# Kernel optimization log

Measured on AMD Instinct MI355X. Metric: run time of the kernel, lower is better.

The kernel has to match this reference:

```python
import jax, jax.numpy as jnp
import numpy as np

T, N, E = 4, 50000, 800000
F, H, C_HID, C_OUT = 256, 128, 512, 2
SLOPE = 11.0 / 48.0  # torch RReLU eval-mode slope = (1/8 + 1/3) / 2


def _topk_pool(x, scorer, k):
    # x: [N, d], scorer: [d, 1] -> [d, k]
    scores = (x @ scorer) / jnp.maximum(jnp.linalg.norm(scorer), 1e-6)  # [N, 1]
    _, idx = jax.lax.top_k(scores[:, 0], k)
    return (x[idx] * jnp.tanh(scores[idx])).T


def _gru_cell(prev_Q, z, Wu, Uu, bu, Wr, Ur, br, Wh, Uh, bh):
    u = jax.nn.sigmoid(Wu @ z + Uu @ prev_Q + bu)
    r = jax.nn.sigmoid(Wr @ z + Ur @ prev_Q + br)
    h_cap = jnp.tanh(Wh @ z + Uh @ (r * prev_Q) + bh)
    return (1.0 - u) * prev_Q + u * h_cap


def _gcn_conv(x, src, dst, W):
    ones = jnp.ones(src.shape[0], x.dtype)
    deg_out = jnp.clip(jax.ops.segment_sum(ones, src, num_segments=N), 1.0)
    deg_in = jnp.clip(jax.ops.segment_sum(ones, dst, num_segments=N), 1.0)
    h = (x * (deg_out ** -0.5)[:, None]) @ W          # project first (out <= in)
    agg = jax.ops.segment_sum(h[src], dst, num_segments=N)
    out = agg * (deg_in ** -0.5)[:, None]
    return jnp.where(out >= 0, out, SLOPE * out)      # RReLU (eval mode)


def setup_inputs() -> dict:
    key = jax.random.key(0)
    ks = jax.random.split(key, 32)
    s = 0.05
    d = {}
    d['feats'] = jax.random.normal(ks[0], (T, N, F), jnp.float32)
    d['edges'] = jax.random.randint(ks[1], (T, 2, E), 0, N)
    d['scorer0'] = jax.random.normal(ks[2], (F, 1), jnp.float32) * s
    d['scorer1'] = jax.random.normal(ks[3], (H, 1), jnp.float32) * s
    d['gcn_W0'] = jax.random.normal(ks[4], (F, H), jnp.float32) * s
    d['gcn_W1'] = jax.random.normal(ks[5], (H, H), jnp.float32) * s
    i = 6
    for g in ('u', 'r', 'h'):
        d[g + '_W0'] = jax.random.normal(ks[i], (F, F), jnp.float32) * s; i += 1
        d[g + '_U0'] = jax.random.normal(ks[i], (F, F), jnp.float32) * s; i += 1
        d[g + '_b0'] = jax.random.normal(ks[i], (F, H), jnp.float32) * s; i += 1
    for g in ('u', 'r', 'h'):
        d[g + '_W1'] = jax.random.normal(ks[i], (H, H), jnp.float32) * s; i += 1
        d[g + '_U1'] = jax.random.normal(ks[i], (H, H), jnp.float32) * s; i += 1
        d[g + '_b1'] = jax.random.normal(ks[i], (H, H), jnp.float32) * s; i += 1
    d['mlp_W1'] = jax.random.normal(ks[i], (H, C_HID), jnp.float32) * s; i += 1
    d['mlp_b1'] = jax.random.normal(ks[i], (C_HID,), jnp.float32) * s; i += 1
    d['mlp_W2'] = jax.random.normal(ks[i], (C_HID, C_OUT), jnp.float32) * s; i += 1
    d['mlp_b2'] = jax.random.normal(ks[i], (C_OUT,), jnp.float32) * s
    return d


def reference(feats, edges, scorer0, scorer1, gcn_W0, gcn_W1,
              u_W0, u_U0, u_b0, r_W0, r_U0, r_b0, h_W0, h_U0, h_b0,
              u_W1, u_U1, u_b1, r_W1, r_U1, r_b1, h_W1, h_U1, h_b1,
              mlp_W1, mlp_b1, mlp_W2, mlp_b2):
    feat_list = [feats[t] for t in range(T)]
    scorers = [scorer0, scorer1]
    gcn_Ws = [gcn_W0, gcn_W1]
    grus = [(u_W0, u_U0, u_b0, r_W0, r_U0, r_b0, h_W0, h_U0, h_b0),
            (u_W1, u_U1, u_b1, r_W1, r_U1, r_b1, h_W1, h_U1, h_b1)]
    for i in range(2):
        W = gcn_Ws[i]
        for t in range(T):
            src, dst = edges[t, 0], edges[t, 1]
            X_tilde = _topk_pool(feat_list[t], scorers[i], H)
            W = _gru_cell(W, X_tilde, *grus[i])
            feat_list[t] = _gcn_conv(feat_list[t], src, dst, W)
    x = feat_list[-1]
    x = jnp.maximum(x @ mlp_W1 + mlp_b1, 0.0)
    return x @ mlp_W2 + mlp_b2
```

## Files before the change

kernel.cpp:

```cpp
#include <hip/hip_runtime.h>

#define NT 4
#define NN 50000
#define NE 800000
#define FD 256
#define HD 128
#define CH 512
#define NBINS 4096
#define CAPC 256
#define RSLOPE 0.22916666666666666f

#define NCH 32
#define CHE (NE / NCH)
#define HALFN 25000
#define WPH 12500
#define WPC 25000

#define C_NORM0 0
#define C_NORM1 1

#define SCAN_BLOCKS 49
#define BT0SZ (HD * 2 * FD)
#define BT1SZ (HD * 2 * HD)

// ... 87 lines not shown
  unsigned short h = f2bf(v);
  hi[idx] = h;
  lo[idx] = f2bf(v - bf2f(h));
}

__device__ __forceinline__ void d_split(int blk, int n, const float* __restrict__ src,
                                        unsigned short* __restrict__ hi,
                                        unsigned short* __restrict__ lo) {
  int idx = blk * 256 + threadIdx.x;
  if (idx >= n) return;
  float v = src[idx];
  unsigned short h = f2bf(v);
  hi[idx] = h;
  lo[idx] = f2bf(v - bf2f(h));
}

__global__ __launch_bounds__(256) void k_startup(
    const float* __restrict__ scorer0, const float* __restrict__ scorer1,
    float* __restrict__ ctlf,
    const float* __restrict__ mlpW1, unsigned short* __restrict__ mW1thi,
    unsigned short* __restrict__ mW1tlo,
    const float* __restrict__ gcnW0, const float* __restrict__ gcnW1,
    unsigned short* __restrict__ bt0hi, unsigned short* __restrict__ bt0lo,
    unsigned short* __restrict__ bt1hi, unsigned short* __restrict__ bt1lo,
    const float* __restrict__ u_W0, const float* __restrict__ u_U0,
    const float* __restrict__ r_W0, const float* __restrict__ r_U0,
    const float* __restrict__ h_W0,
    unsigned short* __restrict__ acat0hi, unsigned short* __restrict__ acat0lo,
    const float* __restrict__ u_W1, const float* __restrict__ u_U1,
    const float* __restrict__ r_W1, const float* __restrict__ r_U1,
    const float* __restrict__ h_W1,
    unsigned short* __restrict__ acat1hi, unsigned short* __restrict__ acat1lo,
    const float* __restrict__ uh0, unsigned short* __restrict__ uh0hi,
    unsigned short* __restrict__ uh0lo,
    const float* __restrict__ uh1, unsigned short* __restrict__ uh1hi,
    unsigned short* __restrict__ uh1lo,
    float* __restrict__ Q0, float* __restrict__ Q1) {
  __shared__ float red[256];
  __shared__ float tile[32][33];
  int b = blockIdx.x;
  if (b == SU_NORM0) { d_norm(scorer0, FD, ctlf, C_NORM0, red); return; }
  if (b == SU_NORM1) { d_norm(scorer1, HD, ctlf, C_NORM1, red); return; }
  if (b < SU_CVT_B) { int r = b - SU_CVT_A; d_cvtT(r & 15, r >> 4, mlpW1, CH, mW1thi, mW1tlo, HD, 0, tile); return; }
  if (b < SU_CVT_C) { int r = b - SU_CVT_B; d_cvtT(r & 3, r >> 2, gcnW0, HD, bt0hi, bt0lo, 2 * FD, FD, tile); return; }
  if (b < SU_CAT0)  { int r = b - SU_CVT_C; d_cvtT(r & 3, r >> 2, gcnW1, HD, bt1hi, bt1lo, 2 * HD, HD, tile); return; }
  if (b < SU_CAT1)  { d_catsplit(b - SU_CAT0, FD, u_W0, u_U0, r_W0, r_U0, h_W0, acat0hi, acat0lo); return; }
  if (b < SU_SPL0)  { d_catsplit(b - SU_CAT1, HD, u_W1, u_U1, r_W1, r_U1, h_W1, acat1hi, acat1lo); return; }
  if (b < SU_SPL1)  { d_split(b - SU_SPL0, FD * FD, uh0, uh0hi, uh0lo); return; }
  if (b < SU_CPQ0)  { d_split(b - SU_SPL1, HD * HD, uh1, uh1hi, uh1lo); return; }
  if (b < SU_CPQ1)  { int i = (b - SU_CPQ0) * 256 + threadIdx.x; ((float4*)Q0)[i] = ((const float4*)gcnW0)[i]; return; }
  { int i = (b - SU_CPQ1) * 256 + threadIdx.x; ((float4*)Q1)[i] = ((const float4*)gcnW1)[i]; }
}

__global__ __launch_bounds__(1024) void k_degC(const int* __restrict__ edges,
                                               unsigned int* __restrict__ chist) {
  __shared__ unsigned int lcnt[WPH];
  int t = blockIdx.y, c = blockIdx.x;
  int tid = threadIdx.x;
  for (int dir = 0; dir < 2; ++dir) {
    const int* E = edges + (size_t)t * 2 * NE + (size_t)dir * NE + (size_t)c * CHE;
    for (int half = 0; half < 2; ++half) {
      for (int i = tid; i < WPH; i += 1024) lcnt[i] = 0;
      __syncthreads();
      int lo = half * HALFN;
      for (int j = tid; j < CHE; j += 1024) {
        int n = E[j] - lo;
        if ((unsigned)n < (unsigned)HALFN)
          atomicAdd(&lcnt[n >> 1], 1u << ((n & 1) * 16));
      }
      __syncthreads();
      unsigned int* dst = chist + (((size_t)dir * NT + t) * NCH + c) * WPC + (size_t)half * WPH;
      for (int i = tid; i < WPH; i += 1024) dst[i] = lcnt[i];
      __syncthreads();
    }
  }
}

__global__ __launch_bounds__(1024) void k_scanB(const unsigned int* __restrict__ chist,
                                                unsigned int* __restrict__ lbase,
                                                float* __restrict__ dor4,
                                                float* __restrict__ din4,
                                                int* __restrict__ rowptr4,
                                                int* __restrict__ bsum4) {
  int t = blockIdx.y;
  int tid = threadIdx.x;
  int g = blockIdx.x * 1024 + tid;
  int lane = tid & 63, wid = tid >> 6;
  int v = 0;
  if (g < NN) {
    int w = g >> 1, sh = (g & 1) * 16;
    const unsigned int* oh = chist + ((size_t)0 * NT + t) * NCH * WPC;
    const unsigned int* ih = chist + ((size_t)1 * NT + t) * NCH * WPC;
    int o = 0;
#pragma unroll
    for (int c = 0; c < NCH; ++c) o += (oh[(size_t)c * WPC + w] >> sh) & 0xffff;
    dor4[t * NN + g] = 1.f / sqrtf((float)max(o, 1));
    int run = 0;
#pragma unroll
    for (int c = 0; c < NCH; ++c) {
      lbase[((size_t)t * NCH + c) * NN + g] = (unsigned int)run;
      run += (ih[(size_t)c * WPC + w] >> sh) & 0xffff;
    }
    v = run;
    din4[t * NN + g] = 1.f / sqrtf((float)max(v, 1));
  }
  int s = v;
  for (int o = 1; o < 64; o <<= 1) {
    int u = __shfl_up(s, o, 64);
    if (lane >= o) s += u;
  }
  __shared__ int ws[16];
  if (lane == 63) ws[wid] = s;
  __syncthreads();
  if (wid == 0 && lane < 16) {
    int u = ws[lane];
    int ss = u;
    for (int o = 1; o < 16; o <<= 1) {
      int w2 = __shfl_up(ss, o, 64);
      if (lane >= o) ss += w2;
    }
    ws[lane] = ss - u;
  }
  __syncthreads();
  int incl = s + ws[wid];
  if (g < NN) rowptr4[(size_t)t * (NN + 1) + g] = incl - v;
  if (tid == 1023) bsum4[t * SCAN_BLOCKS + blockIdx.x] = incl;
}

__global__ __launch_bounds__(1024) void k_scan2b(int* __restrict__ rowptr4,
                                                 const int* __restrict__ bsum4) {
  int t = blockIdx.x;
  int* rowptr = rowptr4 + (size_t)t * (NN + 1);
  const int* bsum = bsum4 + t * SCAN_BLOCKS;
  __shared__ int boff[SCAN_BLOCKS];
  __shared__ int total;
  int tid = threadIdx.x;
  if (tid < 64) {
    int v = (tid < SCAN_BLOCKS) ? bsum[tid] : 0;
    int s = v;
    for (int o = 1; o < 64; o <<= 1) {
      int u = __shfl_up(s, o, 64);
      if (tid >= o) s += u;
    }
    if (tid < SCAN_BLOCKS) boff[tid] = s - v;
    if (tid == SCAN_BLOCKS - 1) total = s;
  }
  __syncthreads();
  for (int i = tid; i < NN; i += 1024) rowptr[i] += boff[i >> 10];
  if (tid == 0) rowptr[NN] = total;
}

__global__ __launch_bounds__(1024) void k_scatC(const int* __restrict__ edges,
                                                const int* __restrict__ rowptr4,
                                                const unsigned int* __restrict__ lbase,
                                                int* __restrict__ srcs4) {
  __shared__ unsigned int lcnt[WPH];
  int t = blockIdx.y, c = blockIdx.x;
  int tid = threadIdx.x;
  const int* srcE = edges + (size_t)t * 2 * NE + (size_t)c * CHE;
  const int* dstE = srcE + NE;
  const int* rowptr = rowptr4 + (size_t)t * (NN + 1);
  const unsigned int* lb = lbase + ((size_t)t * NCH + c) * NN;
  int* srcs = srcs4 + (size_t)t * NE;
  for (int half = 0; half < 2; ++half) {
    for (int i = tid; i < WPH; i += 1024) lcnt[i] = 0;
    __syncthreads();
    int lo = half * HALFN;
    for (int j = tid; j < CHE; j += 1024) {
      int d = dstE[j];
      int n = d - lo;
      if ((unsigned)n < (unsigned)HALFN) {
        unsigned int old = atomicAdd(&lcnt[n >> 1], 1u << ((n & 1) * 16));
        int ord = (int)((old >> ((n & 1) * 16)) & 0xffff);
        int pos = rowptr[d] + (int)lb[d] + ord;
        srcs[pos] = srcE[j];
      }
    }
    __syncthreads();
  }
}

__global__ void k_scores0_all(const float* __restrict__ feats, const float* __restrict__ sc,
                              const float* __restrict__ ctlf, float* __restrict__ scores0) {
  int t = blockIdx.y;
  int w = (blockIdx.x * blockDim.x + threadIdx.x) >> 6;
  int lane = threadIdx.x & 63;
  if (w >= NN) return;
  size_t rowoff = ((size_t)t * NN + w) * FD;
  float4 x = *(const float4*)(feats + rowoff + lane * 4);
  float4 s = *(const float4*)(sc + lane * 4);
  double acc = (double)x.x * s.x + (double)x.y * s.y + (double)x.z * s.z + (double)x.w * s.w;
  for (int m = 32; m > 0; m >>= 1) acc += __shfl_xor(acc, m, 64);
  if (lane == 0) scores0[(size_t)t * NN + w] = (float)(acc / (double)ctlf[C_NORM0]);
}

template <int LOGD>
__global__ __launch_bounds__(1024) void k_pool(const float* __restrict__ Xb, long xStride,
                                               const float* __restrict__ scoresB, int sStride,
                                               unsigned short* __restrict__ bthiB,
                                               unsigned short* __restrict__ btloB,
                                               long btStride, int ldb) {
  const int D = 1 << LOGD;
  int t = blockIdx.x;
  const float* X = Xb + (size_t)t * xStride;
  const float* scores = scoresB + (size_t)t * sStride;
  unsigned short* bthi = bthiB + (size_t)t * btStride;
  unsigned short* btlo = btloB + (size_t)t * btStride;
  __shared__ int hist[NBINS];
  __shared__ int sufT[1024];
  __shared__ float cs[CAPC];
  __shared__ int ci[CAPC];
  __shared__ float stv[HD];
  __shared__ int sidx[HD];
  __shared__ int thrBin, cnt;
  int tid = threadIdx.x;
  for (int i = tid; i < NBINS; i += 1024) hist[i] = 0;
  if (tid == 0) cnt = 0;
  __syncthreads();
  for (int i = tid; i < NN; i += 1024) atomicAdd(&hist[sbin(scores[i])], 1);
  __syncthreads();

  int h0 = hist[4 * tid + 0], h1 = hist[4 * tid + 1];
  int h2 = hist[4 * tid + 2], h3 = hist[4 * tid + 3];
  int l3 = h3, l2 = h2 + l3, l1 = h1 + l2, l0 = h0 + l1;
  sufT[tid] = l0;
  __syncthreads();
  for (int off = 1; off < 1024; off <<= 1) {
    int u = (tid + off < 1024) ? sufT[tid + off] : 0;
    __syncthreads();
    sufT[tid] += u;
    __syncthreads();
  }
  {
    int higher = sufT[tid] - l0;
    int S0 = l0 + higher, S1 = l1 + higher, S2 = l2 + higher, S3 = l3 + higher;
    int S4 = higher;
    if (S3 >= HD && S4 < HD) thrBin = 4 * tid + 3;
    else if (S2 >= HD && S3 < HD) thrBin = 4 * tid + 2;
    else if (S1 >= HD && S2 < HD) thrBin = 4 * tid + 1;
    else if (S0 >= HD && S1 < HD) thrBin = 4 * tid + 0;
  }
  __syncthreads();
  int thr = thrBin;
  for (int i = tid; i < NN; i += 1024) {
    float s = scores[i];
    if (sbin(s) >= thr) {
      int p = atomicAdd(&cnt, 1);
      if (p < CAPC) { cs[p] = s; ci[p] = i; }
    }
  }
  __syncthreads();
  int M = min(cnt, CAPC);
  for (int i = tid; i < CAPC; i += 1024)
    if (i >= M) { cs[i] = -3.4e38f; ci[i] = 0x7fffffff; }
  __syncthreads();
  for (int k = 2; k <= CAPC; k <<= 1) {
    for (int j = k >> 1; j > 0; j >>= 1) {
      int i = tid;
      if (i < CAPC) {
        int l = i ^ j;
        if (l > i) {
          float si = cs[i], sl = cs[l];
          int di = ci[i], dl = ci[l];
          bool lb = (sl > si) || (sl == si && dl < di);
          bool ib = (si > sl) || (si == sl && di < dl);
          bool dir = ((i & k) == 0);
          if (dir ? lb : ib) {
            cs[i] = sl; cs[l] = si; ci[i] = dl; ci[l] = di;
          }
        }
      }
      __syncthreads();
    }
  }
  if (tid < HD) {
    stv[tid] = tanhf(cs[tid]);
    sidx[tid] = ci[tid];
  }
  __syncthreads();
  for (int e4 = tid * 4; e4 < D * HD; e4 += 1024 * 4) {
    int j = e4 >> LOGD, f = e4 & (D - 1);
    float4 x = *(const float4*)&X[(size_t)sidx[j] * D + f];
    float sv = stv[j];
    x.x *= sv; x.y *= sv; x.z *= sv; x.w *= sv;
    ushort4 h, l;
    h.x = f2bf(x.x); l.x = f2bf(x.x - bf2f(h.x));
    h.y = f2bf(x.y); l.y = f2bf(x.y - bf2f(h.y));
    h.z = f2bf(x.z); l.z = f2bf(x.z - bf2f(h.z));
    h.w = f2bf(x.w); l.w = f2bf(x.w - bf2f(h.w));
    *(ushort4*)&bthi[(size_t)j * ldb + f] = h;
    *(ushort4*)&btlo[(size_t)j * ldb + f] = l;
  }
}

__global__ __launch_bounds__(256) void k_gruA(
    const unsigned short* __restrict__ Ahi, const unsigned short* __restrict__ Alo,
    const unsigned short* __restrict__ Bhi, const unsigned short* __restrict__ Blo,
    int d, const float* __restrict__ bu, const float* __restrict__ br,
    const float* __restrict__ bh, const float* __restrict__ Q,
    float* __restrict__ u, float* __restrict__ hz,
    unsigned short* __restrict__ rqThi, unsigned short* __restrict__ rqTlo) {
  __shared__ unsigned short AshH[64 * 32], AshL[64 * 32];
  __shared__ unsigned short BshH[128 * 32], BshL[128 * 32];
  int K = 2 * d;
  int tid = threadIdx.x;
  int lane = tid & 63, wave = tid >> 6;
  int wr = wave >> 1, wc = wave & 1;
  int n0 = blockIdx.x * 64;
  f32x4 acc[2][4];
#pragma unroll
  for (int m = 0; m < 2; ++m)
#pragma unroll
    for (int n = 0; n < 4; ++n) acc[m][n] = (f32x4){0.f, 0.f, 0.f, 0.f};
  int arow = tid >> 2, aseg = tid & 3;
  int as = (aseg ^ (arow & 3)) * 8;
  int kseg = lane >> 4;
  for (int k0 = 0; k0 < K; k0 += 32) {
    __syncthreads();
    {
      size_t off = (size_t)(n0 + arow) * K + k0 + aseg * 8;
      *(bf16x8*)&AshH[arow * 32 + as] = *(const bf16x8*)(Ahi + off);
      *(bf16x8*)&AshL[arow * 32 + as] = *(const bf16x8*)(Alo + off);
    }
#pragma unroll
    for (int h = 0; h < 2; ++h) {
      int id = tid + h * 256;
      int br2 = id >> 2, bseg = id & 3;
      int bs = (bseg ^ (br2 & 3)) * 8;
      size_t off = (size_t)br2 * K + k0 + bseg * 8;
      *(bf16x8*)&BshH[br2 * 32 + bs] = *(const bf16x8*)(Bhi + off);
      *(bf16x8*)&BshL[br2 * 32 + bs] = *(const bf16x8*)(Blo + off);
    }
    __syncthreads();
    bf16x8 ah[2], al[2], bh8[4], bl8[4];
#pragma unroll
    for (int m = 0; m < 2; ++m) {
      int row = wr * 32 + m * 16 + (lane & 15);
      int s = (kseg ^ (row & 3)) * 8;
      ah[m] = *(bf16x8*)&AshH[row * 32 + s];
      al[m] = *(bf16x8*)&AshL[row * 32 + s];
    }
#pragma unroll
    for (int n = 0; n < 4; ++n) {
      int col = wc * 64 + n * 16 + (lane & 15);
// ... 170 lines not shown
    }
#pragma unroll
    for (int h = 0; h < 2; ++h) {
      int id = tid + h * 256;
      int br = id >> 2, bseg = id & 3;
      int bs = (bseg ^ (br & 3)) * 8;
      size_t off = (size_t)br * ldb + k0 + bseg * 8;
      *(bf16x8*)&BshH[br * 32 + bs] = *(const bf16x8*)(Bhi + off);
      *(bf16x8*)&BshL[br * 32 + bs] = *(const bf16x8*)(Blo + off);
    }
    __syncthreads();

    bf16x8 ah[2], al[2], bh[4], bl[4];
#pragma unroll
    for (int m = 0; m < 2; ++m) {
      int row = wr * 32 + m * 16 + (lane & 15);
      int s = (kseg ^ (row & 3)) * 8;
      ah[m] = *(bf16x8*)&AshH[row * 32 + s];
      al[m] = *(bf16x8*)&AshL[row * 32 + s];
    }
#pragma unroll
    for (int n = 0; n < 4; ++n) {
      int col = wc * 64 + n * 16 + (lane & 15);
      int s = (kseg ^ (col & 3)) * 8;
      bh[n] = *(bf16x8*)&BshH[col * 32 + s];
      bl[n] = *(bf16x8*)&BshL[col * 32 + s];
    }
#pragma unroll
    for (int m = 0; m < 2; ++m)
#pragma unroll
      for (int n = 0; n < 4; ++n) {
        acc[m][n] = __builtin_amdgcn_mfma_f32_16x16x32_bf16(ah[m], bh[n], acc[m][n], 0, 0, 0);
        acc[m][n] = __builtin_amdgcn_mfma_f32_16x16x32_bf16(al[m], bh[n], acc[m][n], 0, 0, 0);
        acc[m][n] = __builtin_amdgcn_mfma_f32_16x16x32_bf16(ah[m], bl[n], acc[m][n], 0, 0, 0);
      }
  }

#pragma unroll
  for (int m = 0; m < 2; ++m) {
#pragma unroll
    for (int q = 0; q < 4; ++q) {
      int row = n0 + wr * 32 + m * 16 + (lane >> 4) * 4 + q;
      if (row >= NN) continue;
      float rsv = rs[row];
#pragma unroll
      for (int n = 0; n < 4; ++n) {
        int col = wc * 64 + n * 16 + (lane & 15);
        C[(size_t)row * HD + col] = acc[m][n][q] * rsv;
      }
    }
  }
}

__global__ __launch_bounds__(256) void k_gemm3(
    const unsigned short* __restrict__ Ahi, const unsigned short* __restrict__ Alo, int lda,
    const unsigned short* __restrict__ Bhi, const unsigned short* __restrict__ Blo, int ldb,
    float* __restrict__ C, int ldo, int M, int K,
    const float* __restrict__ rs) {
  __shared__ unsigned short AshH[64 * 32], AshL[64 * 32];
  __shared__ unsigned short BshH[128 * 32], BshL[128 * 32];
  int tid = threadIdx.x;
  int lane = tid & 63, wave = tid >> 6;
  int wr = wave >> 1, wc = wave & 1;
  int n0 = blockIdx.x * 64;
  int c0 = blockIdx.y * 128;
  f32x4 acc[2][4];
#pragma unroll
  for (int m = 0; m < 2; ++m)
#pragma unroll
    for (int n = 0; n < 4; ++n) acc[m][n] = (f32x4){0.f, 0.f, 0.f, 0.f};

  int arow = tid >> 2, aseg = tid & 3;
  int as = (aseg ^ (arow & 3)) * 8;
  int kseg = lane >> 4;

  for (int k0 = 0; k0 < K; k0 += 32) {
    __syncthreads();
    {
      bf16x8 vh = (bf16x8)(short)0, vl = (bf16x8)(short)0;
      int row = n0 + arow;
      if (row < M) {
        size_t off = (size_t)row * lda + k0 + aseg * 8;
        vh = *(const bf16x8*)(Ahi + off);
        vl = *(const bf16x8*)(Alo + off);
      }
      *(bf16x8*)&AshH[arow * 32 + as] = vh;
      *(bf16x8*)&AshL[arow * 32 + as] = vl;
    }
#pragma unroll
    for (int h = 0; h < 2; ++h) {
      int id = tid + h * 256;
      int br = id >> 2, bseg = id & 3;
      int bs = (bseg ^ (br & 3)) * 8;
      size_t off = (size_t)(c0 + br) * ldb + k0 + bseg * 8;
      *(bf16x8*)&BshH[br * 32 + bs] = *(const bf16x8*)(Bhi + off);
      *(bf16x8*)&BshL[br * 32 + bs] = *(const bf16x8*)(Blo + off);
    }
    __syncthreads();

    bf16x8 ah[2], al[2], bh[4], bl[4];
#pragma unroll
    for (int m = 0; m < 2; ++m) {
      int row = wr * 32 + m * 16 + (lane & 15);
      int s = (kseg ^ (row & 3)) * 8;
      ah[m] = *(bf16x8*)&AshH[row * 32 + s];
      al[m] = *(bf16x8*)&AshL[row * 32 + s];
    }
#pragma unroll
    for (int n = 0; n < 4; ++n) {
      int col = wc * 64 + n * 16 + (lane & 15);
      int s = (kseg ^ (col & 3)) * 8;
      bh[n] = *(bf16x8*)&BshH[col * 32 + s];
      bl[n] = *(bf16x8*)&BshL[col * 32 + s];
    }
#pragma unroll
    for (int m = 0; m < 2; ++m)
#pragma unroll
      for (int n = 0; n < 4; ++n) {
        acc[m][n] = __builtin_amdgcn_mfma_f32_16x16x32_bf16(ah[m], bh[n], acc[m][n], 0, 0, 0);
        acc[m][n] = __builtin_amdgcn_mfma_f32_16x16x32_bf16(al[m], bh[n], acc[m][n], 0, 0, 0);
        acc[m][n] = __builtin_amdgcn_mfma_f32_16x16x32_bf16(ah[m], bl[n], acc[m][n], 0, 0, 0);
      }
  }

#pragma unroll
  for (int m = 0; m < 2; ++m) {
#pragma unroll
    for (int q = 0; q < 4; ++q) {
      int row = n0 + wr * 32 + m * 16 + (lane >> 4) * 4 + q;
      if (row >= M) continue;
      float rsv = rs[row];
#pragma unroll
      for (int n = 0; n < 4; ++n) {
        int col = c0 + wc * 64 + n * 16 + (lane & 15);
        C[(size_t)row * ldo + col] = acc[m][n][q] * rsv;
      }
    }
  }
}

__global__ __launch_bounds__(256) void k_gemmMLPagg(
    const float* __restrict__ h, const int* __restrict__ rowptr,
    const int* __restrict__ srcs, const float* __restrict__ din,
    const unsigned short* __restrict__ Bhi, const unsigned short* __restrict__ Blo,
    const float* __restrict__ bias, const float* __restrict__ W2,
    const float* __restrict__ b2, float* __restrict__ out, int M) {
  __shared__ unsigned short AshH[64 * 128], AshL[64 * 128];
  __shared__ unsigned short BshH[128 * 32], BshL[128 * 32];
  __shared__ float osum[64][2];
  int tid = threadIdx.x;
  int lane = tid & 63, wave = tid >> 6;
  int wr = wave >> 1, wc = wave & 1;
  int n0 = blockIdx.x * 64;
  if (tid < 128) ((float*)osum)[tid] = 0.f;

  {
    int row = tid >> 2, seg = tid & 3;
    int grow = n0 + row;
    float a[32];
#pragma unroll
    for (int i = 0; i < 32; ++i) a[i] = 0.f;
    if (grow < M) {
      int beg = rowptr[grow], end = rowptr[grow + 1];
      int c0 = seg * 32;
      for (int e = beg; e < end; ++e) {
        const float* hr = h + (size_t)srcs[e] * HD + c0;
#pragma unroll
        for (int i = 0; i < 8; ++i) {
          float4 v = *(const float4*)(hr + i * 4);
          a[i * 4 + 0] += v.x; a[i * 4 + 1] += v.y;
          a[i * 4 + 2] += v.z; a[i * 4 + 3] += v.w;
        }
      }
      float dn = din[grow];
#pragma unroll
      for (int i = 0; i < 32; ++i) {
        float v = a[i] * dn;
        a[i] = v >= 0.f ? v : RSLOPE * v;
      }
    }
#pragma unroll
    for (int q = 0; q < 4; ++q) {
      int s = seg * 4 + q;
      bf16x8 vh, vl;
#pragma unroll
      for (int j = 0; j < 8; ++j) {
        float v = a[q * 8 + j];
        unsigned short hh = f2bf(v);
        vh[j] = (short)hh;
        vl[j] = (short)f2bf(v - bf2f(hh));
      }
      int sp = (s ^ (row & 15)) * 8;
      *(bf16x8*)&AshH[row * 128 + sp] = vh;
      *(bf16x8*)&AshL[row * 128 + sp] = vl;
    }
  }
  __syncthreads();

  float ps0[2][4], ps1[2][4];
#pragma unroll
  for (int m = 0; m < 2; ++m)
#pragma unroll
    for (int q = 0; q < 4; ++q) { ps0[m][q] = 0.f; ps1[m][q] = 0.f; }

  int kseg = lane >> 4;
  for (int hc = 0; hc < 4; ++hc) {
    f32x4 acc[2][4];
#pragma unroll
    for (int m = 0; m < 2; ++m)
#pragma unroll
      for (int n = 0; n < 4; ++n) acc[m][n] = (f32x4){0.f, 0.f, 0.f, 0.f};
    for (int k0 = 0; k0 < HD; k0 += 32) {
      __syncthreads();
#pragma unroll
      for (int h2 = 0; h2 < 2; ++h2) {
        int id = tid + h2 * 256;
        int br = id >> 2, bseg = id & 3;
        int bs = (bseg ^ (br & 3)) * 8;
        size_t off = (size_t)(hc * 128 + br) * HD + k0 + bseg * 8;
        *(bf16x8*)&BshH[br * 32 + bs] = *(const bf16x8*)(Bhi + off);
        *(bf16x8*)&BshL[br * 32 + bs] = *(const bf16x8*)(Blo + off);
      }
      __syncthreads();
      bf16x8 ah[2], al[2], bh[4], bl[4];
#pragma unroll
      for (int m = 0; m < 2; ++m) {
        int row = wr * 32 + m * 16 + (lane & 15);
        int sg = (k0 >> 3) + kseg;
        int sp = (sg ^ (row & 15)) * 8;
        ah[m] = *(bf16x8*)&AshH[row * 128 + sp];
        al[m] = *(bf16x8*)&AshL[row * 128 + sp];
      }
#pragma unroll
      for (int n = 0; n < 4; ++n) {
        int col = wc * 64 + n * 16 + (lane & 15);
        int s = (kseg ^ (col & 3)) * 8;
        bh[n] = *(bf16x8*)&BshH[col * 32 + s];
        bl[n] = *(bf16x8*)&BshL[col * 32 + s];
      }
#pragma unroll
      for (int m = 0; m < 2; ++m)
#pragma unroll
        for (int n = 0; n < 4; ++n) {
          acc[m][n] = __builtin_amdgcn_mfma_f32_16x16x32_bf16(ah[m], bh[n], acc[m][n], 0, 0, 0);
          acc[m][n] = __builtin_amdgcn_mfma_f32_16x16x32_bf16(al[m], bh[n], acc[m][n], 0, 0, 0);
          acc[m][n] = __builtin_amdgcn_mfma_f32_16x16x32_bf16(ah[m], bl[n], acc[m][n], 0, 0, 0);
        }
    }
#pragma unroll
    for (int n = 0; n < 4; ++n) {
      int col = hc * 128 + wc * 64 + n * 16 + (lane & 15);
      float bcol = bias[col];
      float w20 = W2[2 * col], w21 = W2[2 * col + 1];
#pragma unroll
      for (int m = 0; m < 2; ++m)
#pragma unroll
        for (int q = 0; q < 4; ++q) {
          float v = fmaxf(acc[m][n][q] + bcol, 0.f);
// ... 177 lines not shown
    int id = sidx[j];
    int beg = rowptr[id], end = rowptr[id + 1];
    float ax = 0.f, ay = 0.f;
    for (int e = beg; e < end; ++e) {
      float2 vv = *(const float2*)&h[(size_t)srcs[e] * HD + l2o];
      ax += vv.x; ay += vv.y;
    }
    float dn = din[id];
    ax *= dn; ay *= dn;
    ax = ax >= 0.f ? ax : RSLOPE * ax;
    ay = ay >= 0.f ? ay : RSLOPE * ay;
    float sv = stv[j];
    ax *= sv; ay *= sv;
    unsigned short hx = f2bf(ax), hy = f2bf(ay);
    unsigned short lx = f2bf(ax - bf2f(hx)), ly = f2bf(ay - bf2f(hy));
    *(ushort2*)&bthi[(size_t)j * (2 * HD) + l2o] = make_ushort2(hx, hy);
    *(ushort2*)&btlo[(size_t)j * (2 * HD) + l2o] = make_ushort2(lx, ly);
  }
}

extern "C" void kernel_launch(void* const* d_in, const int* in_sizes, int n_in,
                              void* d_out, int out_size, void* d_ws, size_t ws_size,
                              hipStream_t stream) {
  (void)in_sizes; (void)n_in; (void)out_size; (void)ws_size;
  const float* feats = (const float*)d_in[0];
  const int* edges = (const int*)d_in[1];
  const float* scorer0 = (const float*)d_in[2];
  const float* scorer1 = (const float*)d_in[3];
  const float* gcnW0 = (const float*)d_in[4];
  const float* gcnW1 = (const float*)d_in[5];
  const float* g0[9];
  const float* g1[9];
  for (int i = 0; i < 9; ++i) {
    g0[i] = (const float*)d_in[6 + i];
    g1[i] = (const float*)d_in[15 + i];
  }
  const float* mlpW1 = (const float*)d_in[24];
  const float* mlpB1 = (const float*)d_in[25];
  const float* mlpW2 = (const float*)d_in[26];
  const float* mlpB2 = (const float*)d_in[27];
  float* out = (float*)d_out;

  char* p = (char*)d_ws;
  auto carve = [&p](size_t bytes) {
    void* r = (void*)p;
    p += (bytes + 511) & ~(size_t)511;
    return r;
  };
  float* hbuf4  = (float*)carve((size_t)NT * NN * HD * 4);
  unsigned short* fahi = (unsigned short*)carve((size_t)NN * HD * 2);
  unsigned short* falo = (unsigned short*)carve((size_t)NN * HD * 2);
  int* srcs4   = (int*)carve((size_t)NT * NE * 4);
  int* rowptr4 = (int*)carve((size_t)NT * (NN + 1) * 4);
  unsigned int* chist = (unsigned int*)carve((size_t)2 * NT * NCH * WPC * 4);
  unsigned int* lbase = (unsigned int*)carve((size_t)NT * NCH * NN * 4);
  int* bsum4   = (int*)carve((size_t)NT * SCAN_BLOCKS * 4);
  float* dor4  = (float*)carve((size_t)NT * NN * 4);
  float* din4  = (float*)carve((size_t)NT * NN * 4);
  float* scores0 = (float*)carve((size_t)NT * NN * 4);
  float* scores1_4 = (float*)carve((size_t)NT * NN * 4);
  float* ctlf  = (float*)carve(64 * 4);
  unsigned short* bt0hi = (unsigned short*)carve((size_t)NT * BT0SZ * 2);
  unsigned short* bt0lo = (unsigned short*)carve((size_t)NT * BT0SZ * 2);
  unsigned short* bt1hi = (unsigned short*)carve((size_t)NT * BT1SZ * 2);
  unsigned short* bt1lo = (unsigned short*)carve((size_t)NT * BT1SZ * 2);
  unsigned short* rqThi = (unsigned short*)carve((size_t)HD * FD * 2);
  unsigned short* rqTlo = (unsigned short*)carve((size_t)HD * FD * 2);
  float* ubuf_f = (float*)carve((size_t)FD * HD * 4);
  float* hzbuf  = (float*)carve((size_t)FD * HD * 4);
  unsigned short* acat0hi = (unsigned short*)carve((size_t)3 * FD * 2 * FD * 2);
  unsigned short* acat0lo = (unsigned short*)carve((size_t)3 * FD * 2 * FD * 2);
  unsigned short* acat1hi = (unsigned short*)carve((size_t)3 * HD * 2 * HD * 2);
  unsigned short* acat1lo = (unsigned short*)carve((size_t)3 * HD * 2 * HD * 2);
  unsigned short* uh0hi = (unsigned short*)carve((size_t)FD * FD * 2);
  unsigned short* uh0lo = (unsigned short*)carve((size_t)FD * FD * 2);
  unsigned short* uh1hi = (unsigned short*)carve((size_t)HD * HD * 2);
  unsigned short* uh1lo = (unsigned short*)carve((size_t)HD * HD * 2);
  float* Q0 = (float*)carve((size_t)FD * HD * 4);
  float* Q1 = (float*)carve((size_t)HD * HD * 4);
  unsigned short* mW1thi = (unsigned short*)carve((size_t)CH * HD * 2);
  unsigned short* mW1tlo = (unsigned short*)carve((size_t)CH * HD * 2);

  k_startup<<<SU_TOTAL, 256, 0, stream>>>(
      scorer0, scorer1, ctlf, mlpW1, mW1thi, mW1tlo, gcnW0, gcnW1,
      bt0hi, bt0lo, bt1hi, bt1lo,
      g0[0], g0[1], g0[3], g0[4], g0[6], acat0hi, acat0lo,
      g1[0], g1[1], g1[3], g1[4], g1[6], acat1hi, acat1lo,
      g0[7], uh0hi, uh0lo, g1[7], uh1hi, uh1lo, Q0, Q1);

  k_scores0_all<<<dim3(12500, NT), 256, 0, stream>>>(feats, scorer0, ctlf, scores0);
  k_degC<<<dim3(NCH, NT), 1024, 0, stream>>>(edges, chist);
  k_scanB<<<dim3(SCAN_BLOCKS, NT), 1024, 0, stream>>>(chist, lbase, dor4, din4, rowptr4, bsum4);
  k_scan2b<<<NT, 1024, 0, stream>>>(rowptr4, bsum4);
  k_scatC<<<dim3(NCH, NT), 1024, 0, stream>>>(edges, rowptr4, lbase, srcs4);
  k_pool<8><<<NT, 1024, 0, stream>>>(feats, (long)NN * FD, scores0, NN,
                                     bt0hi, bt0lo, (long)BT0SZ, 2 * FD);

  for (int t = 0; t < NT; ++t) {
    size_t btOff = (size_t)t * BT0SZ;
    size_t btNxt = (size_t)((t + 1) & 3) * BT0SZ;
    k_gruA<<<3 * FD / 64, 256, 0, stream>>>(acat0hi, acat0lo, bt0hi + btOff, bt0lo + btOff,
                                            FD, g0[2], g0[5], g0[8], Q0, ubuf_f, hzbuf,
                                            rqThi, rqTlo);
    k_gruB<<<FD / 64, 256, 0, stream>>>(uh0hi, uh0lo, rqThi, rqTlo, FD, hzbuf, ubuf_f, Q0,
                                        bt0hi + btNxt + FD, bt0lo + btNxt + FD, 2 * FD);
  }

  const int gM = (NN + 63) / 64;

  k_convL0<<<dim3(gM, 1, NT), 256, 0, stream>>>(feats, bt0hi, bt0lo, hbuf4, dor4);

  k_aggB<<<dim3(12500, NT), 256, 0, stream>>>(hbuf4, rowptr4, srcs4, din4,
                                              scorer1, ctlf, scores1_4, fahi, falo);

  k_pool1<<<NT, 1024, 0, stream>>>(hbuf4, rowptr4, srcs4, din4, scores1_4,
                                   bt1hi, bt1lo);

  for (int t = 0; t < NT; ++t) {
    size_t btOff = (size_t)t * BT1SZ;
    size_t btNxt = (size_t)((t + 1) & 3) * BT1SZ;
    k_gruA<<<3 * HD / 64, 256, 0, stream>>>(acat1hi, acat1lo, bt1hi + btOff, bt1lo + btOff,
                                            HD, g1[2], g1[5], g1[8], Q1, ubuf_f, hzbuf,
                                            rqThi, rqTlo);
    k_gruB<<<HD / 64, 256, 0, stream>>>(uh1hi, uh1lo, rqThi, rqTlo, HD, hzbuf, ubuf_f, Q1,
                                        bt1hi + btNxt + HD, bt1lo + btNxt + HD, 2 * HD);
  }

  k_gemm3<<<dim3(gM, 1), 256, 0, stream>>>(fahi, falo, HD,
                                           bt1hi + HD, bt1lo + HD, 2 * HD,
                                           hbuf4, HD, NN, HD, dor4 + (size_t)3 * NN);
  k_gemmMLPagg<<<gM, 256, 0, stream>>>(hbuf4, rowptr4 + (size_t)3 * (NN + 1),
                                       srcs4 + (size_t)3 * NE, din4 + (size_t)3 * NN,
                                       mW1thi, mW1tlo, mlpB1, mlpW2, mlpB2, out, NN);
}
```

Baseline: 1.152 ms.

## Merge preprocessing kernels and fuse final GCN layer into MLP kernel

Degree histogram and scorer-0 dot products now run in one launch, the scan and layer-0 top-k pooling share a second launch, and the block-offset fixup moves into the scatter kernel, which writes a separate finalized rowptr. The last GCN layer now aggregates first (reading the bf16 hi/lo features scaled by the out-degree norm) and then multiplies by the GRU weight inside the MLP kernel. This removes the separate GEMM kernel and its fp32 intermediate round trip. In exchange the aggregation reads split-bf16 inputs instead of fp32 rows and adds a per-edge dor lookup. Merging unrelated work into one grid can also leave imbalanced blocks, such as the single pooling block per timestep.

```diff
diff --git a/kernel.cpp b/kernel.cpp
--- a/kernel.cpp
+++ b/kernel.cpp
@@ -163,139 +163,38 @@
   { int i = (b - SU_CPQ1) * 256 + threadIdx.x; ((float4*)Q1)[i] = ((const float4*)gcnW1)[i]; }
 }
 
-__global__ __launch_bounds__(1024) void k_degC(const int* __restrict__ edges,
-                                               unsigned int* __restrict__ chist) {
+__global__ __launch_bounds__(1024) void k_pre1(const int* __restrict__ edges,
+                                               unsigned int* __restrict__ chist,
+                                               const float* __restrict__ feats,
+                                               const float* __restrict__ sc,
+                                               const float* __restrict__ ctlf,
+                                               float* __restrict__ scores0) {
   __shared__ unsigned int lcnt[WPH];
-  int t = blockIdx.y, c = blockIdx.x;
-  int tid = threadIdx.x;
-  for (int dir = 0; dir < 2; ++dir) {
-    const int* E = edges + (size_t)t * 2 * NE + (size_t)dir * NE + (size_t)c * CHE;
-    for (int half = 0; half < 2; ++half) {
-      for (int i = tid; i < WPH; i += 1024) lcnt[i] = 0;
-      __syncthreads();
-      int lo = half * HALFN;
-      for (int j = tid; j < CHE; j += 1024) {
-        int n = E[j] - lo;
-        if ((unsigned)n < (unsigned)HALFN)
-          atomicAdd(&lcnt[n >> 1], 1u << ((n & 1) * 16));
-      }
-      __syncthreads();
-      unsigned int* dst = chist + (((size_t)dir * NT + t) * NCH + c) * WPC + (size_t)half * WPH;
-      for (int i = tid; i < WPH; i += 1024) dst[i] = lcnt[i];
-      __syncthreads();
-    }
-  }
-}
-
-__global__ __launch_bounds__(1024) void k_scanB(const unsigned int* __restrict__ chist,
-                                                unsigned int* __restrict__ lbase,
-                                                float* __restrict__ dor4,
-                                                float* __restrict__ din4,
-                                                int* __restrict__ rowptr4,
-                                                int* __restrict__ bsum4) {
   int t = blockIdx.y;
   int tid = threadIdx.x;
-  int g = blockIdx.x * 1024 + tid;
-  int lane = tid & 63, wid = tid >> 6;
-  int v = 0;
-  if (g < NN) {
-    int w = g >> 1, sh = (g & 1) * 16;
-    const unsigned int* oh = chist + ((size_t)0 * NT + t) * NCH * WPC;
-    const unsigned int* ih = chist + ((size_t)1 * NT + t) * NCH * WPC;
-    int o = 0;
-#pragma unroll
-    for (int c = 0; c < NCH; ++c) o += (oh[(size_t)c * WPC + w] >> sh) & 0xffff;
-    dor4[t * NN + g] = 1.f / sqrtf((float)max(o, 1));
-    int run = 0;
-#pragma unroll
-    for (int c = 0; c < NCH; ++c) {
-      lbase[((size_t)t * NCH + c) * NN + g] = (unsigned int)run;
-      run += (ih[(size_t)c * WPC + w] >> sh) & 0xffff;
-    }
-    v = run;
-    din4[t * NN + g] = 1.f / sqrtf((float)max(v, 1));
-  }
-  int s = v;
-  for (int o = 1; o < 64; o <<= 1) {
-    int u = __shfl_up(s, o, 64);
-    if (lane >= o) s += u;
-  }
-  __shared__ int ws[16];
-  if (lane == 63) ws[wid] = s;
-  __syncthreads();
-  if (wid == 0 && lane < 16) {
-    int u = ws[lane];
-    int ss = u;
-    for (int o = 1; o < 16; o <<= 1) {
-      int w2 = __shfl_up(ss, o, 64);
-      if (lane >= o) ss += w2;
-    }
-    ws[lane] = ss - u;
-  }
-  __syncthreads();
-  int incl = s + ws[wid];
-  if (g < NN) rowptr4[(size_t)t * (NN + 1) + g] = incl - v;
-  if (tid == 1023) bsum4[t * SCAN_BLOCKS + blockIdx.x] = incl;
-}
-
-__global__ __launch_bounds__(1024) void k_scan2b(int* __restrict__ rowptr4,
-                                                 const int* __restrict__ bsum4) {
-  int t = blockIdx.x;
-  int* rowptr = rowptr4 + (size_t)t * (NN + 1);
-  const int* bsum = bsum4 + t * SCAN_BLOCKS;
-  __shared__ int boff[SCAN_BLOCKS];
-  __shared__ int total;
-  int tid = threadIdx.x;
-  if (tid < 64) {
-    int v = (tid < SCAN_BLOCKS) ? bsum[tid] : 0;
-    int s = v;
-    for (int o = 1; o < 64; o <<= 1) {
-      int u = __shfl_up(s, o, 64);
-      if (tid >= o) s += u;
-    }
-    if (tid < SCAN_BLOCKS) boff[tid] = s - v;
-    if (tid == SCAN_BLOCKS - 1) total = s;
-  }
-  __syncthreads();
-  for (int i = tid; i < NN; i += 1024) rowptr[i] += boff[i >> 10];
-  if (tid == 0) rowptr[NN] = total;
-}
-
-__global__ __launch_bounds__(1024) void k_scatC(const int* __restrict__ edges,
-                                                const int* __restrict__ rowptr4,
-                                                const unsigned int* __restrict__ lbase,
-                                                int* __restrict__ srcs4) {
-  __shared__ unsigned int lcnt[WPH];
-  int t = blockIdx.y, c = blockIdx.x;
-  int tid = threadIdx.x;
-  const int* srcE = edges + (size_t)t * 2 * NE + (size_t)c * CHE;
-  const int* dstE = srcE + NE;
-  const int* rowptr = rowptr4 + (size_t)t * (NN + 1);
-  const unsigned int* lb = lbase + ((size_t)t * NCH + c) * NN;
-  int* srcs = srcs4 + (size_t)t * NE;
-  for (int half = 0; half < 2; ++half) {
-    for (int i = tid; i < WPH; i += 1024) lcnt[i] = 0;
-    __syncthreads();
-    int lo = half * HALFN;
-    for (int j = tid; j < CHE; j += 1024) {
-      int d = dstE[j];
-      int n = d - lo;
-      if ((unsigned)n < (unsigned)HALFN) {
-        unsigned int old = atomicAdd(&lcnt[n >> 1], 1u << ((n & 1) * 16));
-        int ord = (int)((old >> ((n & 1) * 16)) & 0xffff);
-        int pos = rowptr[d] + (int)lb[d] + ord;
-        srcs[pos] = srcE[j];
-      }
-    }
-    __syncthreads();
-  }
-}
-
-__global__ void k_scores0_all(const float* __restrict__ feats, const float* __restrict__ sc,
-                              const float* __restrict__ ctlf, float* __restrict__ scores0) {
-  int t = blockIdx.y;
-  int w = (blockIdx.x * blockDim.x + threadIdx.x) >> 6;
-  int lane = threadIdx.x & 63;
+  if ((int)blockIdx.x < NCH) {
+    int c = blockIdx.x;
+    for (int dir = 0; dir < 2; ++dir) {
+      const int* E = edges + (size_t)t * 2 * NE + (size_t)dir * NE + (size_t)c * CHE;
+      for (int half = 0; half < 2; ++half) {
+        for (int i = tid; i < WPH; i += 1024) lcnt[i] = 0;
+        __syncthreads();
+        int lo = half * HALFN;
+        for (int j = tid; j < CHE; j += 1024) {
+          int n = E[j] - lo;
+          if ((unsigned)n < (unsigned)HALFN)
+            atomicAdd(&lcnt[n >> 1], 1u << ((n & 1) * 16));
+        }
+        __syncthreads();
+        unsigned int* dst = chist + (((size_t)dir * NT + t) * NCH + c) * WPC + (size_t)half * WPH;
+        for (int i = tid; i < WPH; i += 1024) dst[i] = lcnt[i];
+        __syncthreads();
+      }
+    }
+    return;
+  }
+  int w = ((int)blockIdx.x - NCH) * 16 + (tid >> 6);
+  int lane = tid & 63;
   if (w >= NN) return;
   size_t rowoff = ((size_t)t * NN + w) * FD;
   float4 x = *(const float4*)(feats + rowoff + lane * 4);
@@ -305,18 +204,10 @@
   if (lane == 0) scores0[(size_t)t * NN + w] = (float)(acc / (double)ctlf[C_NORM0]);
 }
 
-template <int LOGD>
-__global__ __launch_bounds__(1024) void k_pool(const float* __restrict__ Xb, long xStride,
-                                               const float* __restrict__ scoresB, int sStride,
-                                               unsigned short* __restrict__ bthiB,
-                                               unsigned short* __restrict__ btloB,
-                                               long btStride, int ldb) {
-  const int D = 1 << LOGD;
-  int t = blockIdx.x;
-  const float* X = Xb + (size_t)t * xStride;
-  const float* scores = scoresB + (size_t)t * sStride;
-  unsigned short* bthi = bthiB + (size_t)t * btStride;
-  unsigned short* btlo = btloB + (size_t)t * btStride;
+__device__ void d_pool8(const float* __restrict__ X, const float* __restrict__ scores,
+                        unsigned short* __restrict__ bthi, unsigned short* __restrict__ btlo,
+                        int ldb) {
+  const int D = FD;
   __shared__ int hist[NBINS];
   __shared__ int sufT[1024];
   __shared__ float cs[CAPC];
@@ -390,7 +281,7 @@
   }
   __syncthreads();
   for (int e4 = tid * 4; e4 < D * HD; e4 += 1024 * 4) {
-    int j = e4 >> LOGD, f = e4 & (D - 1);
+    int j = e4 >> 8, f = e4 & (D - 1);
     float4 x = *(const float4*)&X[(size_t)sidx[j] * D + f];
     float sv = stv[j];
     x.x *= sv; x.y *= sv; x.z *= sv; x.w *= sv;
@@ -401,6 +292,115 @@
     h.w = f2bf(x.w); l.w = f2bf(x.w - bf2f(h.w));
     *(ushort4*)&bthi[(size_t)j * ldb + f] = h;
     *(ushort4*)&btlo[(size_t)j * ldb + f] = l;
+  }
+}
+
+__global__ __launch_bounds__(1024) void k_pre2(const unsigned int* __restrict__ chist,
+                                               unsigned int* __restrict__ lbase,
+                                               float* __restrict__ dor4,
+                                               float* __restrict__ din4,
+                                               int* __restrict__ rowptr4,
+                                               int* __restrict__ bsum4,
+                                               const float* __restrict__ feats,
+                                               const float* __restrict__ scores0,
+                                               unsigned short* __restrict__ bt0hi,
+                                               unsigned short* __restrict__ bt0lo) {
+  int t = blockIdx.y;
+  int tid = threadIdx.x;
+  if ((int)blockIdx.x >= SCAN_BLOCKS) {
+    d_pool8(feats + (size_t)t * NN * FD, scores0 + (size_t)t * NN,
+            bt0hi + (size_t)t * BT0SZ, bt0lo + (size_t)t * BT0SZ, 2 * FD);
+    return;
+  }
+  int g = blockIdx.x * 1024 + tid;
+  int lane = tid & 63, wid = tid >> 6;
+  int v = 0;
+  if (g < NN) {
+    int w = g >> 1, sh = (g & 1) * 16;
+    const unsigned int* oh = chist + ((size_t)0 * NT + t) * NCH * WPC;
+    const unsigned int* ih = chist + ((size_t)1 * NT + t) * NCH * WPC;
+    int o = 0;
+#pragma unroll
+    for (int c = 0; c < NCH; ++c) o += (oh[(size_t)c * WPC + w] >> sh) & 0xffff;
+    dor4[t * NN + g] = 1.f / sqrtf((float)max(o, 1));
+    int run = 0;
+#pragma unroll
+    for (int c = 0; c < NCH; ++c) {
+      lbase[((size_t)t * NCH + c) * NN + g] = (unsigned int)run;
+      run += (ih[(size_t)c * WPC + w] >> sh) & 0xffff;
+    }
+    v = run;
+    din4[t * NN + g] = 1.f / sqrtf((float)max(v, 1));
+  }
+  int s = v;
+  for (int o = 1; o < 64; o <<= 1) {
+    int u = __shfl_up(s, o, 64);
+    if (lane >= o) s += u;
+  }
+  __shared__ int ws[16];
+  if (lane == 63) ws[wid] = s;
+  __syncthreads();
+  if (wid == 0 && lane < 16) {
+    int u = ws[lane];
+    int ss = u;
+    for (int o = 1; o < 16; o <<= 1) {
+      int w2 = __shfl_up(ss, o, 64);
+      if (lane >= o) ss += w2;
+    }
+    ws[lane] = ss - u;
+  }
+  __syncthreads();
+  int incl = s + ws[wid];
+  if (g < NN) rowptr4[(size_t)t * (NN + 1) + g] = incl - v;
+  if (tid == 1023) bsum4[t * SCAN_BLOCKS + blockIdx.x] = incl;
+}
+
+__global__ __launch_bounds__(1024) void k_scatF(const int* __restrict__ edges,
+                                                const int* __restrict__ rowptrRaw,
+                                                const int* __restrict__ bsum4,
+                                                const unsigned int* __restrict__ lbase,
+                                                int* __restrict__ srcs4,
+                                                int* __restrict__ rowptrF) {
+  __shared__ unsigned int lcnt[WPH];
+  __shared__ int boff[SCAN_BLOCKS + 1];
+  int t = blockIdx.y, c = blockIdx.x;
+  int tid = threadIdx.x;
+  if (tid < 64) {
+    int v = (tid < SCAN_BLOCKS) ? bsum4[t * SCAN_BLOCKS + tid] : 0;
+    int s = v;
+    for (int o = 1; o < 64; o <<= 1) {
+      int u = __shfl_up(s, o, 64);
+      if (tid >= o) s += u;
+    }
+    if (tid < SCAN_BLOCKS) boff[tid] = s - v;
+    if (tid == SCAN_BLOCKS - 1) boff[SCAN_BLOCKS] = s;
+  }
+  __syncthreads();
+  const int* rowptr = rowptrRaw + (size_t)t * (NN + 1);
+  if (c == 0) {
+    int* rf = rowptrF + (size_t)t * (NN + 1);
+    for (int i = tid; i < NN; i += 1024) rf[i] = rowptr[i] + boff[i >> 10];
+    if (tid == 0) rf[NN] = boff[SCAN_BLOCKS];
+  }
+  const int* srcE = edges + (size_t)t * 2 * NE + (size_t)c * CHE;
+  const int* dstE = srcE + NE;
+  const unsigned int* lb = lbase + ((size_t)t * NCH + c) * NN;
+  int* srcs = srcs4 + (size_t)t * NE;
+  for (int half = 0; half < 2; ++half) {
+    for (int i = tid; i < WPH; i += 1024) lcnt[i] = 0;
+    __syncthreads();
+    int lo = half * HALFN;
+    for (int j = tid; j < CHE; j += 1024) {
+      int d = dstE[j];
+      int n = d - lo;
+      if ((unsigned)n < (unsigned)HALFN) {
+        unsigned int old = atomicAdd(&lcnt[n >> 1], 1u << ((n & 1) * 16));
+        int ord = (int)((old >> ((n & 1) * 16)) & 0xffff);
+        int pos = rowptr[d] + boff[d >> 10] + (int)lb[d] + ord;
+        srcs[pos] = srcE[j];
+      }
+    }
+    __syncthreads();
   }
 }
 
@@ -677,96 +677,11 @@
   }
 }
 
-__global__ __launch_bounds__(256) void k_gemm3(
-    const unsigned short* __restrict__ Ahi, const unsigned short* __restrict__ Alo, int lda,
-    const unsigned short* __restrict__ Bhi, const unsigned short* __restrict__ Blo, int ldb,
-    float* __restrict__ C, int ldo, int M, int K,
-    const float* __restrict__ rs) {
-  __shared__ unsigned short AshH[64 * 32], AshL[64 * 32];
-  __shared__ unsigned short BshH[128 * 32], BshL[128 * 32];
-  int tid = threadIdx.x;
-  int lane = tid & 63, wave = tid >> 6;
-  int wr = wave >> 1, wc = wave & 1;
-  int n0 = blockIdx.x * 64;
-  int c0 = blockIdx.y * 128;
-  f32x4 acc[2][4];
-#pragma unroll
-  for (int m = 0; m < 2; ++m)
-#pragma unroll
-    for (int n = 0; n < 4; ++n) acc[m][n] = (f32x4){0.f, 0.f, 0.f, 0.f};
-
-  int arow = tid >> 2, aseg = tid & 3;
-  int as = (aseg ^ (arow & 3)) * 8;
-  int kseg = lane >> 4;
-
-  for (int k0 = 0; k0 < K; k0 += 32) {
-    __syncthreads();
-    {
-      bf16x8 vh = (bf16x8)(short)0, vl = (bf16x8)(short)0;
-      int row = n0 + arow;
-      if (row < M) {
-        size_t off = (size_t)row * lda + k0 + aseg * 8;
-        vh = *(const bf16x8*)(Ahi + off);
-        vl = *(const bf16x8*)(Alo + off);
-      }
-      *(bf16x8*)&AshH[arow * 32 + as] = vh;
-      *(bf16x8*)&AshL[arow * 32 + as] = vl;
-    }
-#pragma unroll
-    for (int h = 0; h < 2; ++h) {
-      int id = tid + h * 256;
-      int br = id >> 2, bseg = id & 3;
-      int bs = (bseg ^ (br & 3)) * 8;
-      size_t off = (size_t)(c0 + br) * ldb + k0 + bseg * 8;
-      *(bf16x8*)&BshH[br * 32 + bs] = *(const bf16x8*)(Bhi + off);
-      *(bf16x8*)&BshL[br * 32 + bs] = *(const bf16x8*)(Blo + off);
-    }
-    __syncthreads();
-
-    bf16x8 ah[2], al[2], bh[4], bl[4];
-#pragma unroll
-    for (int m = 0; m < 2; ++m) {
-      int row = wr * 32 + m * 16 + (lane & 15);
-      int s = (kseg ^ (row & 3)) * 8;
-      ah[m] = *(bf16x8*)&AshH[row * 32 + s];
-      al[m] = *(bf16x8*)&AshL[row * 32 + s];
-    }
-#pragma unroll
-    for (int n = 0; n < 4; ++n) {
-      int col = wc * 64 + n * 16 + (lane & 15);
-      int s = (kseg ^ (col & 3)) * 8;
-      bh[n] = *(bf16x8*)&BshH[col * 32 + s];
-      bl[n] = *(bf16x8*)&BshL[col * 32 + s];
-    }
-#pragma unroll
-    for (int m = 0; m < 2; ++m)
-#pragma unroll
-      for (int n = 0; n < 4; ++n) {
-        acc[m][n] = __builtin_amdgcn_mfma_f32_16x16x32_bf16(ah[m], bh[n], acc[m][n], 0, 0, 0);
-        acc[m][n] = __builtin_amdgcn_mfma_f32_16x16x32_bf16(al[m], bh[n], acc[m][n], 0, 0, 0);
-        acc[m][n] = __builtin_amdgcn_mfma_f32_16x16x32_bf16(ah[m], bl[n], acc[m][n], 0, 0, 0);
-      }
-  }
-
-#pragma unroll
-  for (int m = 0; m < 2; ++m) {
-#pragma unroll
-    for (int q = 0; q < 4; ++q) {
-      int row = n0 + wr * 32 + m * 16 + (lane >> 4) * 4 + q;
-      if (row >= M) continue;
-      float rsv = rs[row];
-#pragma unroll
-      for (int n = 0; n < 4; ++n) {
-        int col = c0 + wc * 64 + n * 16 + (lane & 15);
-        C[(size_t)row * ldo + col] = acc[m][n][q] * rsv;
-      }
-    }
-  }
-}
-
-__global__ __launch_bounds__(256) void k_gemmMLPagg(
-    const float* __restrict__ h, const int* __restrict__ rowptr,
-    const int* __restrict__ srcs, const float* __restrict__ din,
+__global__ __launch_bounds__(256) void k_mlpFull(
+    const unsigned short* __restrict__ fahi, const unsigned short* __restrict__ falo,
+    const int* __restrict__ rowptr, const int* __restrict__ srcs,
+    const float* __restrict__ dor, const float* __restrict__ din,
+    const unsigned short* __restrict__ Whi, const unsigned short* __restrict__ Wlo, int ldw,
     const unsigned short* __restrict__ Bhi, const unsigned short* __restrict__ Blo,
     const float* __restrict__ bias, const float* __restrict__ W2,
     const float* __restrict__ b2, float* __restrict__ out, int M) {
@@ -777,6 +692,7 @@
   int lane = tid & 63, wave = tid >> 6;
   int wr = wave >> 1, wc = wave & 1;
   int n0 = blockIdx.x * 64;
+  int kseg = lane >> 4;
   if (tid < 128) ((float*)osum)[tid] = 0.f;
 
   {
@@ -789,19 +705,18 @@
       int beg = rowptr[grow], end = rowptr[grow + 1];
       int c0 = seg * 32;
       for (int e = beg; e < end; ++e) {
-        const float* hr = h + (size_t)srcs[e] * HD + c0;
-#pragma unroll
-        for (int i = 0; i < 8; ++i) {
-          float4 v = *(const float4*)(hr + i * 4);
-          a[i * 4 + 0] += v.x; a[i * 4 + 1] += v.y;
-          a[i * 4 + 2] += v.z; a[i * 4 + 3] += v.w;
+        int s = srcs[e];
+        float dv = dor[s];
+        const unsigned short* hh = fahi + (size_t)s * HD + c0;
+        const unsigned short* ll = falo + (size_t)s * HD + c0;
+#pragma unroll
+        for (int i = 0; i < 4; ++i) {
+          bf16x8 h8 = *(const bf16x8*)(hh + i * 8);
+          bf16x8 l8 = *(const bf16x8*)(ll + i * 8);
+#pragma unroll
+          for (int j = 0; j < 8; ++j)
+            a[i * 8 + j] += (bf2f((unsigned short)h8[j]) + bf2f((unsigned short)l8[j])) * dv;
         }
-      }
-      float dn = din[grow];
-#pragma unroll
-      for (int i = 0; i < 32; ++i) {
-        float v = a[i] * dn;
-        a[i] = v >= 0.f ? v : RSLOPE * v;
       }
     }
 #pragma unroll
@@ -822,13 +737,77 @@
   }
   __syncthreads();
 
+  f32x4 acc1[2][4];
+#pragma unroll
+  for (int m = 0; m < 2; ++m)
+#pragma unroll
+    for (int n = 0; n < 4; ++n) acc1[m][n] = (f32x4){0.f, 0.f, 0.f, 0.f};
+  for (int k0 = 0; k0 < HD; k0 += 32) {
+    __syncthreads();
+#pragma unroll
+    for (int h2 = 0; h2 < 2; ++h2) {
+      int id = tid + h2 * 256;
+      int br = id >> 2, bseg = id & 3;
+      int bs = (bseg ^ (br & 3)) * 8;
+      size_t off = (size_t)br * ldw + k0 + bseg * 8;
+      *(bf16x8*)&BshH[br * 32 + bs] = *(const bf16x8*)(Whi + off);
+      *(bf16x8*)&BshL[br * 32 + bs] = *(const bf16x8*)(Wlo + off);
+    }
+    __syncthreads();
+    bf16x8 ah[2], al[2], bh[4], bl[4];
+#pragma unroll
+    for (int m = 0; m < 2; ++m) {
+      int row = wr * 32 + m * 16 + (lane & 15);
+      int sg = (k0 >> 3) + kseg;
+      int sp = (sg ^ (row & 15)) * 8;
+      ah[m] = *(bf16x8*)&AshH[row * 128 + sp];
+      al[m] = *(bf16x8*)&AshL[row * 128 + sp];
+    }
+#pragma unroll
+    for (int n = 0; n < 4; ++n) {
+      int col = wc * 64 + n * 16 + (lane & 15);
+      int s = (kseg ^ (col & 3)) * 8;
+      bh[n] = *(bf16x8*)&BshH[col * 32 + s];
+      bl[n] = *(bf16x8*)&BshL[col * 32 + s];
+    }
+#pragma unroll
+    for (int m = 0; m < 2; ++m)
+#pragma unroll
+      for (int n = 0; n < 4; ++n) {
+        acc1[m][n] = __builtin_amdgcn_mfma_f32_16x16x32_bf16(ah[m], bh[n], acc1[m][n], 0, 0, 0);
+        acc1[m][n] = __builtin_amdgcn_mfma_f32_16x16x32_bf16(al[m], bh[n], acc1[m][n], 0, 0, 0);
+        acc1[m][n] = __builtin_amdgcn_mfma_f32_16x16x32_bf16(ah[m], bl[n], acc1[m][n], 0, 0, 0);
+      }
+  }
+  __syncthreads();
+#pragma unroll
+  for (int m = 0; m < 2; ++m) {
+#pragma unroll
+    for (int q = 0; q < 4; ++q) {
+      int row = wr * 32 + m * 16 + (lane >> 4) * 4 + q;
+      int grow = n0 + row;
+      float dnv = (grow < M) ? din[grow] : 0.f;
+#pragma unroll
+      for (int n = 0; n < 4; ++n) {
+        int col = wc * 64 + n * 16 + (lane & 15);
+        float v = acc1[m][n][q] * dnv;
+        v = v >= 0.f ? v : RSLOPE * v;
+        unsigned short hh = f2bf(v);
+        unsigned short llv = f2bf(v - bf2f(hh));
+        int sp = ((col >> 3) ^ (row & 15)) * 8 + (col & 7);
+        AshH[row * 128 + sp] = hh;
+        AshL[row * 128 + sp] = llv;
+      }
+    }
+  }
+  __syncthreads();
+
   float ps0[2][4], ps1[2][4];
 #pragma unroll
   for (int m = 0; m < 2; ++m)
 #pragma unroll
     for (int q = 0; q < 4; ++q) { ps0[m][q] = 0.f; ps1[m][q] = 0.f; }
 
-  int kseg = lane >> 4;
   for (int hc = 0; hc < 4; ++hc) {
     f32x4 acc[2][4];
 #pragma unroll
@@ -1112,6 +1091,7 @@
   unsigned short* falo = (unsigned short*)carve((size_t)NN * HD * 2);
   int* srcs4   = (int*)carve((size_t)NT * NE * 4);
   int* rowptr4 = (int*)carve((size_t)NT * (NN + 1) * 4);
+  int* rowptrF = (int*)carve((size_t)NT * (NN + 1) * 4);
   unsigned int* chist = (unsigned int*)carve((size_t)2 * NT * NCH * WPC * 4);
   unsigned int* lbase = (unsigned int*)carve((size_t)NT * NCH * NN * 4);
   int* bsum4   = (int*)carve((size_t)NT * SCAN_BLOCKS * 4);
@@ -1148,13 +1128,13 @@
       g1[0], g1[1], g1[3], g1[4], g1[6], acat1hi, acat1lo,
       g0[7], uh0hi, uh0lo, g1[7], uh1hi, uh1lo, Q0, Q1);
 
-  k_scores0_all<<<dim3(12500, NT), 256, 0, stream>>>(feats, scorer0, ctlf, scores0);
-  k_degC<<<dim3(NCH, NT), 1024, 0, stream>>>(edges, chist);
-  k_scanB<<<dim3(SCAN_BLOCKS, NT), 1024, 0, stream>>>(chist, lbase, dor4, din4, rowptr4, bsum4);
-  k_scan2b<<<NT, 1024, 0, stream>>>(rowptr4, bsum4);
-  k_scatC<<<dim3(NCH, NT), 1024, 0, stream>>>(edges, rowptr4, lbase, srcs4);
-  k_pool<8><<<NT, 1024, 0, stream>>>(feats, (long)NN * FD, scores0, NN,
-                                     bt0hi, bt0lo, (long)BT0SZ, 2 * FD);
+  k_pre1<<<dim3(NCH + 3125, NT), 1024, 0, stream>>>(edges, chist, feats, scorer0,
+                                                    ctlf, scores0);
+  k_pre2<<<dim3(SCAN_BLOCKS + 1, NT), 1024, 0, stream>>>(chist, lbase, dor4, din4,
+                                                         rowptr4, bsum4, feats, scores0,
+                                                         bt0hi, bt0lo);
+  k_scatF<<<dim3(NCH, NT), 1024, 0, stream>>>(edges, rowptr4, bsum4, lbase, srcs4,
+                                              rowptrF);
 
   for (int t = 0; t < NT; ++t) {
     size_t btOff = (size_t)t * BT0SZ;
@@ -1170,10 +1150,10 @@
 
   k_convL0<<<dim3(gM, 1, NT), 256, 0, stream>>>(feats, bt0hi, bt0lo, hbuf4, dor4);
 
-  k_aggB<<<dim3(12500, NT), 256, 0, stream>>>(hbuf4, rowptr4, srcs4, din4,
+  k_aggB<<<dim3(12500, NT), 256, 0, stream>>>(hbuf4, rowptrF, srcs4, din4,
                                               scorer1, ctlf, scores1_4, fahi, falo);
 
-  k_pool1<<<NT, 1024, 0, stream>>>(hbuf4, rowptr4, srcs4, din4, scores1_4,
+  k_pool1<<<NT, 1024, 0, stream>>>(hbuf4, rowptrF, srcs4, din4, scores1_4,
                                    bt1hi, bt1lo);
 
   for (int t = 0; t < NT; ++t) {
@@ -1186,10 +1166,10 @@
                                         bt1hi + btNxt + HD, bt1lo + btNxt + HD, 2 * HD);
   }
 
-  k_gemm3<<<dim3(gM, 1), 256, 0, stream>>>(fahi, falo, HD,
-                                           bt1hi + HD, bt1lo + HD, 2 * HD,
-                                           hbuf4, HD, NN, HD, dor4 + (size_t)3 * NN);
-  k_gemmMLPagg<<<gM, 256, 0, stream>>>(hbuf4, rowptr4 + (size_t)3 * (NN + 1),
-                                       srcs4 + (size_t)3 * NE, din4 + (size_t)3 * NN,
-                                       mW1thi, mW1tlo, mlpB1, mlpW2, mlpB2, out, NN);
-}
+  k_mlpFull<<<gM, 256, 0, stream>>>(fahi, falo,
+                                    rowptrF + (size_t)3 * (NN + 1),
+                                    srcs4 + (size_t)3 * NE,
+                                    dor4 + (size_t)3 * NN, din4 + (size_t)3 * NN,
+                                    bt1hi + HD, bt1lo + HD, 2 * HD,
+                                    mW1thi, mW1tlo, mlpB1, mlpW2, mlpB2, out, NN);
+}
```

Result: no change. 1.143 ms (-0.8%).
